# Performance work log

Measured on AMD Instinct MI355X. Metric: run time of the kernel, lower is better.

The kernel has to match this reference:

```python
import jax, jax.numpy as jnp
import numpy as np

B, S, E, D = 4, 4096, 512, 64

def setup_inputs() -> dict:
    key = jax.random.key(0)
    kx, kq, kk, kv = jax.random.split(key, 4)
    # xavier_normal std = sqrt(2/(E+D))
    std = float(np.sqrt(2.0 / (E + D)))
    return {
        "x": jax.random.normal(kx, (B, S, E), dtype=jnp.float32),
        "WQ": jax.random.normal(kq, (E, D), dtype=jnp.float32) * std,
        "WK": jax.random.normal(kk, (E, D), dtype=jnp.float32) * std,
        "WV": jax.random.normal(kv, (E, D), dtype=jnp.float32) * std,
    }

def reference(x, WQ, WK, WV):
    # Single-head causal attention; NOTE: scale uses embedding_size (E), as in source.
    Q = x @ WQ  # [B,S,D]
    K = x @ WK
    V = x @ WV
    scale = 1.0 / jnp.sqrt(jnp.float32(E))
    scores = jnp.einsum("bqd,bkd->bqk", Q, K) * scale  # [B,S,S]
    s = scores.shape[1]
    causal = jnp.tril(jnp.ones((s, s), dtype=bool))  # True = keep
    scores = jnp.where(causal[None, :, :], scores, -jnp.inf)
    attn = jax.nn.softmax(scores, axis=2)
    return jnp.einsum("bqk,bkd->bqd", attn, V)
```

## Files before the change

### kernel.cpp

```cpp
#include <hip/hip_runtime.h>
#include <hip/hip_bf16.h>

namespace {
constexpr int B = 4, S = 4096, E = 512, D = 64;
constexpr int NS = 4;
constexpr float SCALE_LOG2E = 0.04419417382415922f * 1.4426950408889634f;

typedef __bf16 bf16x8 __attribute__((ext_vector_type(8)));
typedef float floatx4 __attribute__((ext_vector_type(4)));
}

__global__ __launch_bounds__(256) void prep_wt(
    const float* __restrict__ WQ, const float* __restrict__ WK,
    const float* __restrict__ WV, __bf16* __restrict__ Wt)
{
    __shared__ __bf16 tile[64][72];
    const int t = threadIdx.x;
    const int mat = blockIdx.x >> 3;
    const int k0  = (blockIdx.x & 7) * 64;
    const float* W = (mat == 0) ? WQ : (mat == 1) ? WK : WV;
    #pragma unroll
    for (int i = 0; i < 16; ++i) {
        const int k = (t >> 6) + i * 4;
        tile[t & 63][k] = (__bf16)W[(k0 + k) * 64 + (t & 63)];
    }
    __syncthreads();
    #pragma unroll
    for (int i = 0; i < 2; ++i) {
        const int u = t + 256 * i;
        const int n = u >> 3, kseg = (u & 7) * 8;
        *(bf16x8*)(Wt + (mat * 64 + n) * 512 + k0 + kseg) =
            *(const bf16x8*)&tile[n][kseg];
    }
}

__global__ __launch_bounds__(256) void qkv_mfma(
    const float* __restrict__ x, const __bf16* __restrict__ Wt,
    __bf16* __restrict__ Qb, __bf16* __restrict__ Kb, __bf16* __restrict__ Vt)
{
    __shared__ __bf16 xs[32][72];
    __shared__ __bf16 ws[192][72];
    __shared__ __bf16 vsh[64][40];

    const int t = threadIdx.x;
    const int wave = t >> 6, lane = t & 63, quad = lane >> 4, l16 = lane & 15;
    const long row0 = (long)blockIdx.x * 32;

    floatx4 acc[2][3];
    #pragma unroll
    for (int m = 0; m < 2; ++m)
        #pragma unroll
        for (int n = 0; n < 3; ++n) acc[m][n] = (floatx4){0.f, 0.f, 0.f, 0.f};

    for (int kc = 0; kc < 8; ++kc) {
        __syncthreads();
        {
            const int r = t >> 3, c = (t & 7) * 8;
            const float* src = x + (row0 + r) * E + kc * 64 + c;
            float4 f0 = *(const float4*)src;
            float4 f1 = *(const float4*)(src + 4);
            bf16x8 v;
            v[0] = (__bf16)f0.x; v[1] = (__bf16)f0.y; v[2] = (__bf16)f0.z; v[3] = (__bf16)f0.w;
            v[4] = (__bf16)f1.x; v[5] = (__bf16)f1.y; v[6] = (__bf16)f1.z; v[7] = (__bf16)f1.w;
            *(bf16x8*)&xs[r][c] = v;
        }
        {
            #pragma unroll
            for (int i = 0; i < 6; ++i) {
                const int c = t + 256 * i;
                const int n = c >> 3, seg = (c & 7) * 8;
                *(bf16x8*)&ws[n][seg] = *(const bf16x8*)(Wt + n * 512 + kc * 64 + seg);
            }
        }
        __syncthreads();

        bf16x8 aa[2][2];
        #pragma unroll
        for (int m = 0; m < 2; ++m)
            #pragma unroll
            for (int ch = 0; ch < 2; ++ch)
                aa[m][ch] = *(const bf16x8*)&xs[m * 16 + l16][ch * 32 + quad * 8];
        #pragma unroll
        for (int ns = 0; ns < 3; ++ns) {
            #pragma unroll
            for (int ch = 0; ch < 2; ++ch) {
                bf16x8 bb = *(const bf16x8*)&ws[wave * 48 + ns * 16 + l16][ch * 32 + quad * 8];
                #pragma unroll
                for (int m = 0; m < 2; ++m)
                    acc[m][ns] = __builtin_amdgcn_mfma_f32_16x16x32_bf16(aa[m][ch], bb, acc[m][ns], 0, 0, 0);
            }
        }
    }

    const long bb_ = row0 >> 12;
    const int s0 = (int)(row0 & 4095);
    #pragma unroll
    for (int ns = 0; ns < 3; ++ns) {
        const int g = wave * 3 + ns;
        const int mat = g >> 2;
        const int col = (g & 3) * 16 + l16;
        #pragma unroll
        for (int m = 0; m < 2; ++m) {
            if (mat < 2) {
                __bf16* Out = (mat == 0) ? Qb : Kb;
                #pragma unroll
                for (int r = 0; r < 4; ++r)
                    Out[(row0 + m * 16 + quad * 4 + r) * 64 + col] = (__bf16)acc[m][ns][r];
            } else {
                __bf16 p[4];
                #pragma unroll
                for (int r = 0; r < 4; ++r) p[r] = (__bf16)acc[m][ns][r];
                *(unsigned long long*)&vsh[col][m * 16 + quad * 4] = *(unsigned long long*)p;
            }
        }
    }
    __syncthreads();
    {
        const int d = t >> 2, seg = (t & 3) * 8;
        bf16x8 v = *(const bf16x8*)&vsh[d][seg];
        *(bf16x8*)(Vt + (bb_ * 64 + d) * 4096 + s0 + seg) = v;
    }
}

__global__ __launch_bounds__(256) void attn_kernel(
    const __bf16* __restrict__ Qg, const __bf16* __restrict__ Kg,
    const __bf16* __restrict__ Vt, __bf16* __restrict__ Opart,
    float* __restrict__ Lpart)
{
    __shared__ __bf16 Ks[64][72];
    __shared__ __bf16 Vts[64][72];
    __shared__ __bf16 Ps[4][16][72];

    const int qt = 63 - blockIdx.x;
    const int c  = blockIdx.y;
    const int b  = blockIdx.z;
    const int q0 = qt * 64;
    const int t  = threadIdx.x;
    const int wave = t >> 6, lane = t & 63, quad = lane >> 4, l16 = lane & 15;

    const int nkt    = qt + 1;
    const int cs     = (nkt + NS - 1) / NS;
    const int kstart = c * cs;
    const int kend   = min(kstart + cs, nkt);

    const __bf16* qrow = Qg + ((long)(b * S + q0 + wave * 16 + l16)) * D;
    bf16x8 aq[2];
    aq[0] = *(const bf16x8*)(qrow + quad * 8);
    aq[1] = *(const bf16x8*)(qrow + 32 + quad * 8);

    bf16x8 ones;
    #pragma unroll
    for (int j = 0; j < 8; ++j) ones[j] = (__bf16)1.0f;

    floatx4 o[4];
    #pragma unroll
    for (int i = 0; i < 4; ++i) o[i] = (floatx4){0.f, 0.f, 0.f, 0.f};
    floatx4 lsum = (floatx4){0.f, 0.f, 0.f, 0.f};

    const int srow = t >> 2;
    const int sseg = (t & 3) * 16;

    for (int ktg = kstart; ktg < kend; ++ktg) {
        const int kbase = ktg * 64;
        __syncthreads();
        {
            const __bf16* ks = Kg + ((long)(b * S + kbase + srow)) * D + sseg;
            bf16x8 k0 = *(const bf16x8*)ks;
            bf16x8 k1 = *(const bf16x8*)(ks + 8);
            *(bf16x8*)&Ks[srow][sseg]     = k0;
            *(bf16x8*)&Ks[srow][sseg + 8] = k1;
            const __bf16* vs = Vt + ((long)(b * 64 + srow)) * 4096 + kbase + sseg;
            bf16x8 v0 = *(const bf16x8*)vs;
            bf16x8 v1 = *(const bf16x8*)(vs + 8);
            *(bf16x8*)&Vts[srow][sseg]     = v0;
            *(bf16x8*)&Vts[srow][sseg + 8] = v1;
        }
        __syncthreads();

        floatx4 sf[4];
        #pragma unroll
        for (int ns = 0; ns < 4; ++ns) {
            floatx4 cacc = (floatx4){0.f, 0.f, 0.f, 0.f};
            #pragma unroll
            for (int ch = 0; ch < 2; ++ch) {
                bf16x8 bk = *(const bf16x8*)&Ks[ns * 16 + l16][ch * 32 + quad * 8];
                cacc = __builtin_amdgcn_mfma_f32_16x16x32_bf16(aq[ch], bk, cacc, 0, 0, 0);
            }
            sf[ns] = cacc;
        }

        if (ktg == nkt - 1) {
            #pragma unroll
            for (int ns = 0; ns < 4; ++ns) {
                const int key = kbase + ns * 16 + l16;
                #pragma unroll
                for (int r = 0; r < 4; ++r) {
                    const int qr = q0 + wave * 16 + quad * 4 + r;
                    if (key > qr) sf[ns][r] = -1e30f;
                }
            }
        }

        #pragma unroll
        for (int ns = 0; ns < 4; ++ns)
            #pragma unroll
            for (int r = 0; r < 4; ++r) {
                float p = __builtin_amdgcn_exp2f(sf[ns][r] * SCALE_LOG2E);
                Ps[wave][quad * 4 + r][ns * 16 + l16] = (__bf16)p;
            }

        bf16x8 ap[2];
        ap[0] = *(const bf16x8*)&Ps[wave][l16][quad * 8];
        ap[1] = *(const bf16x8*)&Ps[wave][l16][32 + quad * 8];

        lsum = __builtin_amdgcn_mfma_f32_16x16x32_bf16(ap[0], ones, lsum, 0, 0, 0);
        lsum = __builtin_amdgcn_mfma_f32_16x16x32_bf16(ap[1], ones, lsum, 0, 0, 0);

        #pragma unroll
        for (int dsb = 0; dsb < 4; ++dsb) {
            floatx4 cacc = o[dsb];
            #pragma unroll
            for (int ch = 0; ch < 2; ++ch) {
                bf16x8 bv = *(const bf16x8*)&Vts[dsb * 16 + l16][ch * 32 + quad * 8];
                cacc = __builtin_amdgcn_mfma_f32_16x16x32_bf16(ap[ch], bv, cacc, 0, 0, 0);
            }
            o[dsb] = cacc;
        }
    }

    const long rbase = (long)c * (B * S) + (long)b * S + q0 + wave * 16;
    #pragma unroll
    for (int dsb = 0; dsb < 4; ++dsb)
        #pragma unroll
        for (int r = 0; r < 4; ++r)
            Opart[(rbase + quad * 4 + r) * 64 + dsb * 16 + l16] = (__bf16)o[dsb][r];
    if (l16 == 0) {
        #pragma unroll
        for (int r = 0; r < 4; ++r)
            Lpart[rbase + quad * 4 + r] = lsum[r];
    }
}

__global__ __launch_bounds__(256) void combine_kernel(
    const __bf16* __restrict__ Opart, const float* __restrict__ Lpart,
    float* __restrict__ Og)
{
    const int idx = blockIdx.x * 256 + threadIdx.x;
    const int row = idx >> 3, seg = (idx & 7) * 8;
    float acc[8] = {0, 0, 0, 0, 0, 0, 0, 0};
    float l = 0.f;
    #pragma unroll
    for (int c = 0; c < NS; ++c) {
        bf16x8 ov = *(const bf16x8*)(Opart + ((long)c * (B * S) + row) * 64 + seg);
        l += Lpart[(long)c * (B * S) + row];
        #pragma unroll
        for (int j = 0; j < 8; ++j) acc[j] += (float)ov[j];
    }
    const float invl = 1.f / l;
    float* dst = Og + (long)row * 64 + seg;
    float4 o0 = {acc[0] * invl, acc[1] * invl, acc[2] * invl, acc[3] * invl};
    float4 o1 = {acc[4] * invl, acc[5] * invl, acc[6] * invl, acc[7] * invl};
    *(float4*)dst = o0;
    *(float4*)(dst + 4) = o1;
}

extern "C" void kernel_launch(void* const* d_in, const int* in_sizes, int n_in,
                              void* d_out, int out_size, void* d_ws, size_t ws_size,
                              hipStream_t stream)
{
    const float* x  = (const float*)d_in[0];
    const float* WQ = (const float*)d_in[1];
    const float* WK = (const float*)d_in[2];
    const float* WV = (const float*)d_in[3];
    float* out = (float*)d_out;

    __bf16* Qb = (__bf16*)d_ws;
    __bf16* Kb = Qb + (size_t)B * S * D;
    __bf16* Vt = Kb + (size_t)B * S * D;
    __bf16* Wt = Vt + (size_t)B * S * D;
    __bf16* Opart = Wt + (size_t)3 * E * D;
    float*  Lpart = (float*)(Opart + (size_t)NS * B * S * D);

    prep_wt<<<dim3(24), 256, 0, stream>>>(WQ, WK, WV, Wt);
    qkv_mfma<<<dim3((B * S) / 32), 256, 0, stream>>>(x, Wt, Qb, Kb, Vt);
    attn_kernel<<<dim3(S / 64, NS, B), 256, 0, stream>>>(Qb, Kb, Vt, Opart, Lpart);
    combine_kernel<<<dim3((B * S * 8) / 256), 256, 0, stream>>>(Opart, Lpart, out);
}
```

Before: 128.5 us.

## Register-prefetch next tiles in QKV and attention loops; double split count

The QKV projection and attention loops now load the next chunk's global data (x/W tiles, K/V tiles) into registers before computing on the current shared-memory tile. The aim is to overlap global memory latency with MFMA work. NS (the key-split count) rises from 4 to 8, which adds parallelism but also more partial results to combine. Register pressure increases, which may lower occupancy.

```diff
diff --git a/kernel.cpp b/kernel.cpp
--- a/kernel.cpp
+++ b/kernel.cpp
@@ -3,7 +3,7 @@
 
 namespace {
 constexpr int B = 4, S = 4096, E = 512, D = 64;
-constexpr int NS = 4;
+constexpr int NS = 8;
 constexpr float SCALE_LOG2E = 0.04419417382415922f * 1.4426950408889634f;
 
 typedef __bf16 bf16x8 __attribute__((ext_vector_type(8)));
@@ -46,33 +46,54 @@
     const int wave = t >> 6, lane = t & 63, quad = lane >> 4, l16 = lane & 15;
     const long row0 = (long)blockIdx.x * 32;
 
+    const int xrr = t >> 3, xcc = (t & 7) * 8;
+
     floatx4 acc[2][3];
     #pragma unroll
     for (int m = 0; m < 2; ++m)
         #pragma unroll
         for (int n = 0; n < 3; ++n) acc[m][n] = (floatx4){0.f, 0.f, 0.f, 0.f};
+
+    float4 xf0, xf1;
+    bf16x8 wf[6];
+    {
+        const float* src = x + (row0 + xrr) * E + xcc;
+        xf0 = *(const float4*)src;
+        xf1 = *(const float4*)(src + 4);
+        #pragma unroll
+        for (int i = 0; i < 6; ++i) {
+            const int c = t + 256 * i;
+            wf[i] = *(const bf16x8*)(Wt + (c >> 3) * 512 + (c & 7) * 8);
+        }
+    }
 
     for (int kc = 0; kc < 8; ++kc) {
         __syncthreads();
         {
-            const int r = t >> 3, c = (t & 7) * 8;
-            const float* src = x + (row0 + r) * E + kc * 64 + c;
-            float4 f0 = *(const float4*)src;
-            float4 f1 = *(const float4*)(src + 4);
             bf16x8 v;
-            v[0] = (__bf16)f0.x; v[1] = (__bf16)f0.y; v[2] = (__bf16)f0.z; v[3] = (__bf16)f0.w;
-            v[4] = (__bf16)f1.x; v[5] = (__bf16)f1.y; v[6] = (__bf16)f1.z; v[7] = (__bf16)f1.w;
-            *(bf16x8*)&xs[r][c] = v;
-        }
-        {
+            v[0] = (__bf16)xf0.x; v[1] = (__bf16)xf0.y;
+            v[2] = (__bf16)xf0.z; v[3] = (__bf16)xf0.w;
+            v[4] = (__bf16)xf1.x; v[5] = (__bf16)xf1.y;
+            v[6] = (__bf16)xf1.z; v[7] = (__bf16)xf1.w;
+            *(bf16x8*)&xs[xrr][xcc] = v;
             #pragma unroll
             for (int i = 0; i < 6; ++i) {
                 const int c = t + 256 * i;
-                const int n = c >> 3, seg = (c & 7) * 8;
-                *(bf16x8*)&ws[n][seg] = *(const bf16x8*)(Wt + n * 512 + kc * 64 + seg);
+                *(bf16x8*)&ws[c >> 3][(c & 7) * 8] = wf[i];
             }
         }
         __syncthreads();
+
+        if (kc < 7) {
+            const float* src = x + (row0 + xrr) * E + (kc + 1) * 64 + xcc;
+            xf0 = *(const float4*)src;
+            xf1 = *(const float4*)(src + 4);
+            #pragma unroll
+            for (int i = 0; i < 6; ++i) {
+                const int c = t + 256 * i;
+                wf[i] = *(const bf16x8*)(Wt + (c >> 3) * 512 + (kc + 1) * 64 + (c & 7) * 8);
+            }
+        }
 
         bf16x8 aa[2][2];
         #pragma unroll
@@ -160,22 +181,33 @@
     const int srow = t >> 2;
     const int sseg = (t & 3) * 16;
 
+    bf16x8 kf0, kf1, vf0, vf1;
+    if (kstart < kend) {
+        const __bf16* ks = Kg + ((long)(b * S + kstart * 64 + srow)) * D + sseg;
+        kf0 = *(const bf16x8*)ks;
+        kf1 = *(const bf16x8*)(ks + 8);
+        const __bf16* vs = Vt + ((long)(b * 64 + srow)) * 4096 + kstart * 64 + sseg;
+        vf0 = *(const bf16x8*)vs;
+        vf1 = *(const bf16x8*)(vs + 8);
+    }
+
     for (int ktg = kstart; ktg < kend; ++ktg) {
         const int kbase = ktg * 64;
         __syncthreads();
-        {
-            const __bf16* ks = Kg + ((long)(b * S + kbase + srow)) * D + sseg;
-            bf16x8 k0 = *(const bf16x8*)ks;
-            bf16x8 k1 = *(const bf16x8*)(ks + 8);
-            *(bf16x8*)&Ks[srow][sseg]     = k0;
-            *(bf16x8*)&Ks[srow][sseg + 8] = k1;
-            const __bf16* vs = Vt + ((long)(b * 64 + srow)) * 4096 + kbase + sseg;
-            bf16x8 v0 = *(const bf16x8*)vs;
-            bf16x8 v1 = *(const bf16x8*)(vs + 8);
-            *(bf16x8*)&Vts[srow][sseg]     = v0;
-            *(bf16x8*)&Vts[srow][sseg + 8] = v1;
-        }
+        *(bf16x8*)&Ks[srow][sseg]      = kf0;
+        *(bf16x8*)&Ks[srow][sseg + 8]  = kf1;
+        *(bf16x8*)&Vts[srow][sseg]     = vf0;
+        *(bf16x8*)&Vts[srow][sseg + 8] = vf1;
         __syncthreads();
+
+        if (ktg + 1 < kend) {
+            const __bf16* ks = Kg + ((long)(b * S + kbase + 64 + srow)) * D + sseg;
+            kf0 = *(const bf16x8*)ks;
+            kf1 = *(const bf16x8*)(ks + 8);
+            const __bf16* vs = Vt + ((long)(b * 64 + srow)) * 4096 + kbase + 64 + sseg;
+            vf0 = *(const bf16x8*)vs;
+            vf1 = *(const bf16x8*)(vs + 8);
+        }
 
         floatx4 sf[4];
         #pragma unroll
```

After: 120.1 us. -6.5%, faster.
